# Performance work log

Hardware: AMD Instinct MI355X
Metric: run time of the kernel (lower is better)

The kernel has to match this reference:

```python
import jax, jax.numpy as jnp
import numpy as np

N_NODES = 50000
N_EDGES = 500000
NEG_SLOPE = 0.2  # PyG GATConv default leaky_relu slope
EPS = 1e-16


def gat_conv(x, src, dst, W, a_src, a_dst, b, heads, ch):
    """PyG-style GATConv (concat=True), self-loops assumed already in src/dst."""
    n = x.shape[0]
    h = (x @ W).reshape(n, heads, ch)                      # [N,H,C]
    alpha_s = jnp.sum(h * a_src, axis=-1)                  # [N,H]
    alpha_d = jnp.sum(h * a_dst, axis=-1)                  # [N,H]
    e = jax.nn.leaky_relu(alpha_s[src] + alpha_d[dst], NEG_SLOPE)  # [E,H]
    m = jax.ops.segment_max(e, dst, num_segments=n)        # [N,H] segment softmax (stable)
    m = jnp.where(jnp.isfinite(m), m, 0.0)
    ex = jnp.exp(e - m[dst])
    den = jax.ops.segment_sum(ex, dst, num_segments=n)
    alpha = ex / (den[dst] + EPS)                          # [E,H]
    msg = h[src] * alpha[..., None]                        # [E,H,C] gather->weight
    out = jax.ops.segment_sum(msg, dst, num_segments=n)    # [N,H,C] scatter-add
    return out.reshape(n, heads * ch) + b


def setup_inputs() -> dict:
    key = jax.random.key(0)
    ks = jax.random.split(key, 11)
    s = 0.05
    return {
        "edge_index": jax.random.randint(ks[0], (2, N_EDGES), 0, N_NODES, dtype=jnp.int32),
        "batch_size": 8,
        "node_emb": jax.random.normal(ks[1], (N_NODES, 64), jnp.float32),
        "W1": jax.random.normal(ks[2], (64, 512), jnp.float32) * s,
        "att_src1": jax.random.normal(ks[3], (4, 128), jnp.float32) * s,
        "att_dst1": jax.random.normal(ks[4], (4, 128), jnp.float32) * s,
        "b1": jax.random.normal(ks[5], (512,), jnp.float32) * s,
        "W2": jax.random.normal(ks[6], (512, 256), jnp.float32) * s,
        "att_src2": jax.random.normal(ks[7], (1, 256), jnp.float32) * s,
        "att_dst2": jax.random.normal(ks[8], (1, 256), jnp.float32) * s,
        "b2": jax.random.normal(ks[9], (256,), jnp.float32) * s,
    }


def reference(edge_index, batch_size, node_emb, W1, att_src1, att_dst1, b1,
              W2, att_src2, att_dst2, b2):
    # add self-loops (PyG GATConv default add_self_loops=True)
    loops = jnp.arange(N_NODES, dtype=edge_index.dtype)
    src = jnp.concatenate([edge_index[0], loops])
    dst = jnp.concatenate([edge_index[1], loops])
    x = gat_conv(node_emb, src, dst, W1, att_src1, att_dst1, b1, heads=4, ch=128)
    x = jax.nn.elu(x)  # dropout inactive at eval
    x = gat_conv(x, src, dst, W2, att_src2, att_dst2, b2, heads=1, ch=256)
    g = jnp.mean(x, axis=0, keepdims=True)                 # [1, 256]
    return jnp.broadcast_to(g, (batch_size, g.shape[1]))
```

## Files before the change

kernel.cpp:

```cpp
#include <hip/hip_runtime.h>
#include <cstdint>

#define N_NODES 50000
#define N_EDGES 500000
#define ET (N_NODES + N_EDGES)
#define WSB 256
#define EBLK 2149
#define NEBLK 12500

typedef unsigned short u16;
typedef unsigned int   u32;
typedef __attribute__((ext_vector_type(8))) short short8;
typedef __attribute__((ext_vector_type(4))) float f32x4;

__device__ __forceinline__ float bf2f(u16 s) { return __uint_as_float((u32)s << 16); }
__device__ __forceinline__ u16 f2bf(float f) {
  u32 u = __float_as_uint(f);
  u32 r = (u + 0x7FFFu + ((u >> 16) & 1u)) >> 16;
  return (u16)r;
}
__device__ __forceinline__ void unpack8(uint4 u, float* f) {
  f[0] = __uint_as_float(u.x << 16); f[1] = __uint_as_float(u.x & 0xffff0000u);
  f[2] = __uint_as_float(u.y << 16); f[3] = __uint_as_float(u.y & 0xffff0000u);
  f[4] = __uint_as_float(u.z << 16); f[5] = __uint_as_float(u.z & 0xffff0000u);
  f[6] = __uint_as_float(u.w << 16); f[7] = __uint_as_float(u.w & 0xffff0000u);
}
__device__ __forceinline__ float lrelu(float v) { return v >= 0.f ? v : 0.2f * v; }

__device__ __forceinline__ int detect_fp32(const u16* __restrict__ ne) {
  int lane = threadIdx.x & 63;
  int bad = 0;
  #pragma unroll
  for (int j = 0; j < 2; ++j) {
    float v = fabsf(bf2f(ne[lane * 2 + j * 128]));
    bad += (!(v < 16.0f)) ? 1 : 0;
  }
  #pragma unroll
  for (int off = 32; off >= 1; off >>= 1) bad += __shfl_xor(bad, off, 64);
  return bad > 16;
}

__global__ __launch_bounds__(256) void k_prep(const int* __restrict__ ei,
                                              int* __restrict__ deg,
                                              const void* __restrict__ ne_src,
                                              u16* __restrict__ ne_b,
                                              const void* __restrict__ w1src,
                                              u16* __restrict__ W1t,
                                              const void* __restrict__ w2src,
                                              u16* __restrict__ W2t,
                                              const void* s0, const void* s1,
                                              const void* s2, const void* s3,
                                              const void* s4, const void* s5,
                                              float* d0, float* d1, float* d2,
                                              float* d3, float* d4, float* d5) {
  int b = blockIdx.x, tid = threadIdx.x;
  if (b < EBLK) {
    int e = b * 256 + tid;
    if (e < ET) {
      int d = (e < N_EDGES) ? ei[N_EDGES + e] : (e - N_EDGES);
      atomicAdd(&deg[d], 1);
    }
    return;
  }
  int fp32 = detect_fp32((const u16*)ne_src);
  b -= EBLK;
  if (b < NEBLK) {
    int i = b * 256 + tid;
    ne_b[i] = fp32 ? f2bf(((const float*)ne_src)[i]) : ((const u16*)ne_src)[i];
    return;
  }
  b -= NEBLK;
  if (b < 640) {
    int i = b * 256 + tid;
    if (i < 32768) {
      int n = i >> 6, k = i & 63;
      W1t[i] = fp32 ? f2bf(((const float*)w1src)[k * 512 + n])
                    : ((const u16*)w1src)[k * 512 + n];
    } else {
      int j = i - 32768;
      int n = j >> 9, k = j & 511;
      W2t[j] = fp32 ? f2bf(((const float*)w2src)[k * 256 + n])
                    : ((const u16*)w2src)[k * 256 + n];
    }
    return;
  }
  b -= 640;
  {
    int i = b * 256 + tid;
    const void* s; float* d; int j;
    if      (i < 512)  { s = s0; d = d0; j = i; }
    else if (i < 1024) { s = s1; d = d1; j = i - 512; }
    else if (i < 1536) { s = s2; d = d2; j = i - 1024; }
    else if (i < 1792) { s = s3; d = d3; j = i - 1536; }
    else if (i < 2048) { s = s4; d = d4; j = i - 1792; }
    else if (i < 2304) { s = s5; d = d5; j = i - 2048; }
    else return;
    d[j] = fp32 ? ((const float*)s)[j] : bf2f(((const u16*)s)[j]);
  }
}

__global__ void k_vab(const u16* __restrict__ W1t,
                      const float* __restrict__ as1v, const float* __restrict__ ad1v,
                      float* __restrict__ va_s, float* __restrict__ va_d,
                      const u16* __restrict__ W2t,
                      const float* __restrict__ as2v, const float* __restrict__ ad2v,
                      float* __restrict__ va2_s, float* __restrict__ va2_d) {
  if (blockIdx.x == 0) {
    int t = threadIdx.x;
    int h = t >> 6, k = t & 63;
    float s = 0.f, d = 0.f;
    for (int c = 0; c < 128; ++c) {
      float w = bf2f(W1t[(size_t)(h * 128 + c) * 64 + k]);
      s = fmaf(as1v[h * 128 + c], w, s);
      d = fmaf(ad1v[h * 128 + c], w, d);
    }
    va_s[t] = s;
    va_d[t] = d;
  } else {
    int k = (blockIdx.x - 1) * 256 + threadIdx.x;
    if (k >= 512) return;
    float s = 0.f, d = 0.f;
    for (int c = 0; c < 256; ++c) {
      float w = bf2f(W2t[(size_t)c * 512 + k]);
      s = fmaf(as2v[c], w, s);
      d = fmaf(ad2v[c], w, d);
    }
    va2_s[k] = s;
    va2_d[k] = d;
  }
}

__global__ __launch_bounds__(1024) void k_partial(const int* __restrict__ deg,
                                                  int* __restrict__ excl,
                                                  int* __restrict__ btot) {
  __shared__ int wsum[16];
  int tid = threadIdx.x;
  int i = blockIdx.x * 1024 + tid;
  int v = (i < N_NODES) ? deg[i] : 0;
  int lane = tid & 63, wid = tid >> 6;
  int incl = v;
  #pragma unroll
  for (int off = 1; off < 64; off <<= 1) {
    int t = __shfl_up(incl, off, 64);
    if (lane >= off) incl += t;
  }
  if (lane == 63) wsum[wid] = incl;
  __syncthreads();
  int prefix = 0;
  for (int w = 0; w < wid; ++w) prefix += wsum[w];
  if (i < N_NODES) excl[i] = prefix + incl - v;
  if (tid == 1023) btot[blockIdx.x] = prefix + incl;
}

__global__ void k_bases(const int* __restrict__ btot, int* __restrict__ bbase,
                        int* __restrict__ row_off, int nb) {
  int lane = threadIdx.x;
  int v = (lane < nb) ? btot[lane] : 0;
  int incl = v;
  #pragma unroll
  for (int off = 1; off < 64; off <<= 1) {
    int t = __shfl_up(incl, off, 64);
    if (lane >= off) incl += t;
  }
  if (lane < nb) bbase[lane] = incl - v;
  if (lane == 0) row_off[N_NODES] = ET;
}

__global__ __launch_bounds__(1024) void k_add(int* __restrict__ row_off,
                                              int* __restrict__ cursor,
                                              const int* __restrict__ bbase) {
  int i = blockIdx.x * 1024 + threadIdx.x;
  if (i < N_NODES) {
    int r = row_off[i] + bbase[blockIdx.x];
    row_off[i] = r;
    cursor[i] = r;
  }
}

__global__ __launch_bounds__(256) void k_scal(const int* __restrict__ ei,
                                              int* __restrict__ cursor,
                                              u16* __restrict__ srcs,
                                              const u16* __restrict__ ne_b,
                                              const float* __restrict__ va_s,
                                              const float* __restrict__ va_d,
                                              float* __restrict__ as_o,
                                              float* __restrict__ ad_o) {
  int b = blockIdx.x;
  if (b < EBLK) {
    int e = b * 256 + threadIdx.x;
    if (e >= ET) return;
    int s, d;
    if (e < N_EDGES) { s = ei[e]; d = ei[N_EDGES + e]; }
    else { s = d = e - N_EDGES; }
    int pos = atomicAdd(&cursor[d], 1);
    srcs[pos] = (u16)s;
    return;
  }
  b -= EBLK;
  int wid = threadIdx.x >> 6, lane = threadIdx.x & 63;
  int n = b * 4 + wid;
  if (n >= N_NODES) return;
  int h = lane >> 4, il = lane & 15;
  u32 u2[2];
  *(uint2*)u2 = *(const uint2*)(ne_b + (size_t)n * 64 + il * 4);
  float f[4];
  f[0] = bf2f((u16)u2[0]); f[1] = bf2f((u16)(u2[0] >> 16));
  f[2] = bf2f((u16)u2[1]); f[3] = bf2f((u16)(u2[1] >> 16));
  float4 vs = *(const float4*)(va_s + h * 64 + il * 4);
  float4 vd = *(const float4*)(va_d + h * 64 + il * 4);
  float s = f[0] * vs.x + f[1] * vs.y + f[2] * vs.z + f[3] * vs.w;
  float d = f[0] * vd.x + f[1] * vd.y + f[2] * vd.z + f[3] * vd.w;
  #pragma unroll
  for (int off = 8; off >= 1; off >>= 1) {
    s += __shfl_xor(s, off, 64);
    d += __shfl_xor(d, off, 64);
  }
  if (il == 0) { as_o[n * 4 + h] = s; ad_o[n * 4 + h] = d; }
}

#define LSTR 40
#define CPAD 136
__global__ __launch_bounds__(256, 6) void k_gemm_l1(const u16* __restrict__ aggne,
                                                    const u16* __restrict__ W1t,
                                                    const float* __restrict__ b1f,
                                                    const float* __restrict__ va2_s,
                                                    const float* __restrict__ va2_d,
                                                    u16* __restrict__ x2,
                                                    float* __restrict__ as2,
                                                    float* __restrict__ ad2, int M) {
  __shared__ __align__(16) u16 smem[64 * CPAD];
  u16* As = smem;
  u16* Bs = smem + 64 * LSTR;
  const int tid = threadIdx.x;
  const int lane = tid & 63, wid = tid >> 6;
  const int wr = (wid >> 1) * 32, wc = (wid & 1) * 64;
  const int m = lane & 15, q = lane >> 4;
  const int row0 = blockIdx.x * 64, head = blockIdx.y;
  const u16* Bt = W1t + (size_t)head * 128 * 64;
  f32x4 acc[2][4] = {};
  #pragma unroll
  for (int kk = 0; kk < 64; kk += 32) {
    {
      int row = tid >> 2, ch = (tid & 3) * 8;
      uint4 u = make_uint4(0, 0, 0, 0);
      int gr = row0 + row;
      if (gr < M) u = *(const uint4*)(aggne + (size_t)gr * 256 + head * 64 + kk + ch);
      *(uint4*)(As + row * LSTR + ch) = u;
    }
    #pragma unroll
    for (int i = 0; i < 2; ++i) {
      int v = tid + i * 256;
      int row = v >> 2, ch = (v & 3) * 8;
      uint4 u = *(const uint4*)(Bt + (size_t)row * 64 + kk + ch);
      *(uint4*)(Bs + row * LSTR + ch) = u;
    }
    __syncthreads();
    short8 af[2], bfr[4];
    #pragma unroll
    for (int t = 0; t < 2; ++t)
      af[t]  = *(const short8*)(As + (wr + t * 16 + m) * LSTR + q * 8);
    #pragma unroll
    for (int t = 0; t < 4; ++t)
      bfr[t] = *(const short8*)(Bs + (wc + t * 16 + m) * LSTR + q * 8);
    #pragma unroll
    for (int mt = 0; mt < 2; ++mt)
      #pragma unroll
      for (int nt = 0; nt < 4; ++nt)
        acc[mt][nt] = __builtin_amdgcn_mfma_f32_16x16x32_bf16(
            af[mt], bfr[nt], acc[mt][nt], 0, 0, 0);
    __syncthreads();
  }
  u16* Cs = smem;
  #pragma unroll
  for (int mt = 0; mt < 2; ++mt) {
    #pragma unroll
    for (int nt = 0; nt < 4; ++nt) {
      int lc = wc + nt * 16 + m;
      float bias = b1f[head * 128 + lc];
      #pragma unroll
      for (int r = 0; r < 4; ++r) {
        float v = acc[mt][nt][r] + bias;
        v = v > 0.f ? v : (__expf(v) - 1.0f);
        Cs[(wr + mt * 16 + q * 4 + r) * CPAD + lc] = f2bf(v);
      }
    }
  }
  __syncthreads();
  int row = tid >> 2, qt = tid & 3;
  int gr = row0 + row;
  if (gr < M) {
    const u16* src = Cs + row * CPAD + qt * 32;
    int cb = head * 128 + qt * 32;
    float s = 0.f, d = 0.f;
    #pragma unroll
    for (int i = 0; i < 4; ++i) {
      uint4 u = *(const uint4*)(src + i * 8);
      *(uint4*)(x2 + (size_t)gr * 512 + cb + i * 8) = u;
      float f[8];
      unpack8(u, f);
      const float* pvs = va2_s + cb + i * 8;
      const float* pvd = va2_d + cb + i * 8;
      #pragma unroll
      for (int j = 0; j < 8; ++j) {
        s = fmaf(f[j], pvs[j], s);
        d = fmaf(f[j], pvd[j], d);
      }
    }
    s += __shfl_xor(s, 1, 64);
    d += __shfl_xor(d, 1, 64);
    s += __shfl_xor(s, 2, 64);
    d += __shfl_xor(d, 2, 64);
    if (qt == 0) {
      atomicAdd(&as2[gr], s);
      atomicAdd(&ad2[gr], d);
    }
  }
}

__global__ __launch_bounds__(256) void k_fagg1(const int* __restrict__ row_off,
                                               const u16* __restrict__ srcs,
                                               const u16* __restrict__ ne_b,
                                               const float* __restrict__ as1,
                                               const float* __restrict__ ad1,
                                               u16* __restrict__ aggne) {
  int wid = threadIdx.x >> 6, lane = threadIdx.x & 63;
  int n = blockIdx.x * 4 + wid;
  if (n >= N_NODES) return;
  int start = row_off[n], end = row_off[n + 1];
  int g = lane >> 4, il = lane & 15;
  float adn_g = ad1[n * 4 + g];
  float sum = 0.f;
  for (int e0 = start; e0 < end; e0 += 16) {
    int e = e0 + il;
    if (e < end) sum += __expf(lrelu(as1[(int)srcs[e] * 4 + g] + adn_g));
  }
  #pragma unroll
  for (int off = 8; off >= 1; off >>= 1) sum += __shfl_xor(sum, off, 64);
  float inv = 1.0f / (sum + 1e-16f);
  float i_[4], d_[4];
  #pragma unroll
  for (int h = 0; h < 4; ++h) {
    i_[h] = __shfl(inv, h * 16, 64);
    d_[h] = __shfl(adn_g, h * 16, 64);
  }
  float acc[4] = {};
  for (int e0 = start; e0 < end; e0 += 64) {
    int lim = end - e0; if (lim > 64) lim = 64;
    int es = e0 + lane;
    int sreg = (int)srcs[es < end ? es : end - 1];
    float4 a = *(const float4*)(as1 + sreg * 4);
    float wreg[4];
    wreg[0] = __expf(lrelu(a.x + d_[0])) * i_[0];
    wreg[1] = __expf(lrelu(a.y + d_[1])) * i_[1];
    wreg[2] = __expf(lrelu(a.z + d_[2])) * i_[2];
    wreg[3] = __expf(lrelu(a.w + d_[3])) * i_[3];
    int j = 0;
    for (; j + 3 < lim; j += 4) {
      int sa = __shfl(sreg, j, 64),     sb = __shfl(sreg, j + 1, 64);
      int sc = __shfl(sreg, j + 2, 64), sd = __shfl(sreg, j + 3, 64);
      float f0 = bf2f(ne_b[(size_t)sa * 64 + lane]);
      float f1 = bf2f(ne_b[(size_t)sb * 64 + lane]);
      float f2 = bf2f(ne_b[(size_t)sc * 64 + lane]);
      float f3 = bf2f(ne_b[(size_t)sd * 64 + lane]);
      #pragma unroll
      for (int h = 0; h < 4; ++h) {
        acc[h] = fmaf(__shfl(wreg[h], j, 64), f0, acc[h]);
        acc[h] = fmaf(__shfl(wreg[h], j + 1, 64), f1, acc[h]);
        acc[h] = fmaf(__shfl(wreg[h], j + 2, 64), f2, acc[h]);
        acc[h] = fmaf(__shfl(wreg[h], j + 3, 64), f3, acc[h]);
      }
    }
    for (; j < lim; ++j) {
      int sa = __shfl(sreg, j, 64);
      float f0 = bf2f(ne_b[(size_t)sa * 64 + lane]);
      #pragma unroll
      for (int h = 0; h < 4; ++h)
        acc[h] = fmaf(__shfl(wreg[h], j, 64), f0, acc[h]);
    }
  }
  #pragma unroll
  for (int h = 0; h < 4; ++h)
    aggne[(size_t)n * 256 + h * 64 + lane] = f2bf(acc[h]);
}

__global__ __launch_bounds__(256) void k_nodew(const int* __restrict__ row_off,
                                               const u16* __restrict__ srcs,
                                               const float* __restrict__ as2,
                                               const float* __restrict__ ad2,
                                               float* __restrict__ c) {
  int wid = threadIdx.x >> 6, lane = threadIdx.x & 63;
  int n = blockIdx.x * 4 + wid;
  if (n >= N_NODES) return;
  int start = row_off[n], end = row_off[n + 1];
  int deg = end - start;
  float adn = ad2[n];
  if (deg <= 64) {
    int e = start + (lane < deg ? lane : 0);
    int s = (int)srcs[e];
    float ex = (lane < deg) ? __expf(lrelu(as2[s] + adn)) : 0.f;
    float sum = ex;
    #pragma unroll
    for (int off = 32; off >= 1; off >>= 1) sum += __shfl_xor(sum, off, 64);
    float w = ex / (sum + 1e-16f);
    if (lane < deg) atomicAdd(&c[s], w);
  } else {
    float sum = 0.f;
    for (int e = start + lane; e < end; e += 64)
      sum += __expf(lrelu(as2[(int)srcs[e]] + adn));
    #pragma unroll
    for (int off = 32; off >= 1; off >>= 1) sum += __shfl_xor(sum, off, 64);
    float inv = 1.0f / (sum + 1e-16f);
    for (int e = start + lane; e < end; e += 64) {
      int s = (int)srcs[e];
      float w = __expf(lrelu(as2[s] + adn)) * inv;
      atomicAdd(&c[s], w);
    }
  }
}

__global__ __launch_bounds__(256) void k_wsum(const u16* __restrict__ x2,
                                              const float* __restrict__ c,
                                              float* __restrict__ s_vec) {
  __shared__ float part[4][512];
  int wid = threadIdx.x >> 6, lane = threadIdx.x & 63;
  int wglob = blockIdx.x * 4 + wid;
  float acc[8] = {};
  int n = wglob;
  for (; n + WSB * 4 < N_NODES; n += WSB * 8) {
    int n2 = n + WSB * 4;
    float c0 = c[n], c1 = c[n2];
    uint4 u0 = *(const uint4*)(x2 + (size_t)n * 512 + lane * 8);
    uint4 u1 = *(const uint4*)(x2 + (size_t)n2 * 512 + lane * 8);
    float f0[8], f1[8];
    unpack8(u0, f0); unpack8(u1, f1);
    #pragma unroll
    for (int j = 0; j < 8; ++j) {
      acc[j] = fmaf(c0, f0[j], acc[j]);
      acc[j] = fmaf(c1, f1[j], acc[j]);
    }
  }
  if (n < N_NODES) {
    float c0 = c[n];
    uint4 u0 = *(const uint4*)(x2 + (size_t)n * 512 + lane * 8);
    float f0[8];
    unpack8(u0, f0);
    #pragma unroll
    for (int j = 0; j < 8; ++j) acc[j] = fmaf(c0, f0[j], acc[j]);
  }
  #pragma unroll
  for (int j = 0; j < 8; ++j) part[wid][lane * 8 + j] = acc[j];
  __syncthreads();
  int t = threadIdx.x;
  float v0 = part[0][t] + part[1][t] + part[2][t] + part[3][t];
  float v1 = part[0][t + 256] + part[1][t + 256] + part[2][t + 256] + part[3][t + 256];
  atomicAdd(&s_vec[t], v0);
  atomicAdd(&s_vec[t + 256], v1);
}

__global__ __launch_bounds__(256) void k_tinyfinal(const float* __restrict__ s_vec,
                                                   const u16* __restrict__ W2t,
                                                   const float* __restrict__ b2f,
                                                   float* __restrict__ out,
                                                   int out_size) {
  int wid = threadIdx.x >> 6, lane = threadIdx.x & 63;
  int cbase = blockIdx.x * 64 + wid * 16;
  float sv[8];
  #pragma unroll
  for (int j = 0; j < 8; ++j) sv[j] = s_vec[lane * 8 + j];
  for (int i = 0; i < 16; ++i) {
    int cc = cbase + i;
    uint4 u = *(const uint4*)(W2t + (size_t)cc * 512 + lane * 8);
    float f[8];
    unpack8(u, f);
    float p = 0.f;
    #pragma unroll
    for (int j = 0; j < 8; ++j) p = fmaf(sv[j], f[j], p);
    #pragma unroll
    for (int off = 32; off >= 1; off >>= 1) p += __shfl_xor(p, off, 64);
    if (lane == 0) {
      float val = p * (1.0f / (float)N_NODES) + b2f[cc];
      for (int o = cc; o < out_size; o += 256) out[o] = val;
    }
  }
}

extern "C" void kernel_launch(void* const* d_in, const int* in_sizes, int n_in,
                              void* d_out, int out_size, void* d_ws, size_t ws_size,
                              hipStream_t stream) {
  (void)in_sizes; (void)n_in; (void)ws_size;
  const int* edge_index = (const int*)d_in[0];
  float* out = (float*)d_out;

  char* w = (char*)d_ws;
  size_t off = 0;
  auto alloc = [&](size_t bytes) -> void* {
    void* p = w + off;
    off += (bytes + 255) & ~(size_t)255;
    return p;
  };
  u16*   ne_b    = (u16*)  alloc((size_t)N_NODES * 64 * 2);
  u16*   W1t     = (u16*)  alloc(32768 * 2);
  u16*   W2t     = (u16*)  alloc(131072 * 2);
  float* as1v    = (float*)alloc(512 * 4);
  float* ad1v    = (float*)alloc(512 * 4);
  float* b1f     = (float*)alloc(512 * 4);
  float* as2v    = (float*)alloc(256 * 4);
  float* ad2v    = (float*)alloc(256 * 4);
  float* b2f     = (float*)alloc(256 * 4);
  float* va_s    = (float*)alloc(256 * 4);
  float* va_d    = (float*)alloc(256 * 4);
  float* va2_s   = (float*)alloc(512 * 4);
  float* va2_d   = (float*)alloc(512 * 4);
  u16*   aggne   = (u16*)  alloc((size_t)N_NODES * 256 * 2);
  u16*   x2      = (u16*)  alloc((size_t)N_NODES * 512 * 2);
  float* as1     = (float*)alloc((size_t)N_NODES * 4 * 4);
  float* ad1     = (float*)alloc((size_t)N_NODES * 4 * 4);
  size_t z0 = off;
  float* as2     = (float*)alloc((size_t)N_NODES * 4);
  float* ad2     = (float*)alloc((size_t)N_NODES * 4);
  float* cwt     = (float*)alloc((size_t)N_NODES * 4);
  float* s_vec   = (float*)alloc(512 * 4);
  int*   deg     = (int*)  alloc((size_t)N_NODES * 4);
  size_t z1 = off;
  int*   row_off = (int*)  alloc((size_t)(N_NODES + 1) * 4);
  int*   cursor  = (int*)  alloc((size_t)N_NODES * 4);
  u16*   srcs    = (u16*)  alloc((size_t)ET * 2);
  int*   btot    = (int*)  alloc(64 * 4);
  int*   bbase   = (int*)  alloc(64 * 4);

  hipMemsetAsync(w + z0, 0, z1 - z0, stream);

  k_prep<<<EBLK + NEBLK + 640 + 9, 256, 0, stream>>>(
      edge_index, deg, d_in[2], ne_b, d_in[3], W1t, d_in[7], W2t,
      d_in[4], d_in[5], d_in[6], d_in[8], d_in[9], d_in[10],
      as1v, ad1v, b1f, as2v, ad2v, b2f);
  k_vab<<<3, 256, 0, stream>>>(W1t, as1v, ad1v, va_s, va_d,
                               W2t, as2v, ad2v, va2_s, va2_d);

  k_partial<<<49, 1024, 0, stream>>>(deg, row_off, btot);
  k_bases  <<<1, 64, 0, stream>>>(btot, bbase, row_off, 49);
  k_add    <<<49, 1024, 0, stream>>>(row_off, cursor, bbase);

  k_scal<<<EBLK + (N_NODES + 3) / 4, 256, 0, stream>>>(
      edge_index, cursor, srcs, ne_b, va_s, va_d, as1, ad1);

  k_fagg1<<<(N_NODES + 3) / 4, 256, 0, stream>>>(row_off, srcs, ne_b, as1, ad1, aggne);
  dim3 gl1((N_NODES + 63) / 64, 4);
  k_gemm_l1<<<gl1, 256, 0, stream>>>(aggne, W1t, b1f, va2_s, va2_d, x2, as2, ad2,
                                     N_NODES);

  k_nodew<<<(N_NODES + 3) / 4, 256, 0, stream>>>(row_off, srcs, as2, ad2, cwt);
  k_wsum<<<WSB, 256, 0, stream>>>(x2, cwt, s_vec);
  k_tinyfinal<<<4, 256, 0, stream>>>(s_vec, W2t, b2f, out, out_size);
}
```

Before: 309.0 us.

## Loop over heads inside GEMM block and drop atomics for layer-2 scores

The layer-1 GEMM kernel now runs one block per 64-row tile and loops over all four heads, loading the full 256-wide A tile into shared memory once instead of using a separate grid dimension per head. The per-node layer-2 attention scores are accumulated in registers across heads and written directly, so the atomicAdds go away and the as2/ad2 buffers move out of the memset range. In exchange, shared memory per block grows to about 68KB and each block does four times the work over a quarter of the blocks. That can lower occupancy and adds more syncthreads barriers per block.

Result: slower. 324.3 us (+5.0%).

```diff
diff --git a/kernel.cpp b/kernel.cpp
--- a/kernel.cpp
+++ b/kernel.cpp
@@ -218,102 +218,107 @@
   if (il == 0) { as_o[n * 4 + h] = s; ad_o[n * 4 + h] = d; }
 }
 
-#define LSTR 40
+#define ASTR 264
+#define BSTR 72
 #define CPAD 136
-__global__ __launch_bounds__(256, 6) void k_gemm_l1(const u16* __restrict__ aggne,
-                                                    const u16* __restrict__ W1t,
-                                                    const float* __restrict__ b1f,
-                                                    const float* __restrict__ va2_s,
-                                                    const float* __restrict__ va2_d,
-                                                    u16* __restrict__ x2,
-                                                    float* __restrict__ as2,
-                                                    float* __restrict__ ad2, int M) {
-  __shared__ __align__(16) u16 smem[64 * CPAD];
-  u16* As = smem;
-  u16* Bs = smem + 64 * LSTR;
+__global__ __launch_bounds__(256) void k_gemm_l1(const u16* __restrict__ aggne,
+                                                 const u16* __restrict__ W1t,
+                                                 const float* __restrict__ b1f,
+                                                 const float* __restrict__ va2_s,
+                                                 const float* __restrict__ va2_d,
+                                                 u16* __restrict__ x2,
+                                                 float* __restrict__ as2,
+                                                 float* __restrict__ ad2, int M) {
+  __shared__ __align__(16) u16 As[64 * ASTR];
+  __shared__ __align__(16) u16 Bs[128 * BSTR];
+  __shared__ __align__(16) u16 Cs[64 * CPAD];
   const int tid = threadIdx.x;
   const int lane = tid & 63, wid = tid >> 6;
   const int wr = (wid >> 1) * 32, wc = (wid & 1) * 64;
   const int m = lane & 15, q = lane >> 4;
-  const int row0 = blockIdx.x * 64, head = blockIdx.y;
-  const u16* Bt = W1t + (size_t)head * 128 * 64;
-  f32x4 acc[2][4] = {};
-  #pragma unroll
-  for (int kk = 0; kk < 64; kk += 32) {
-    {
-      int row = tid >> 2, ch = (tid & 3) * 8;
-      uint4 u = make_uint4(0, 0, 0, 0);
-      int gr = row0 + row;
-      if (gr < M) u = *(const uint4*)(aggne + (size_t)gr * 256 + head * 64 + kk + ch);
-      *(uint4*)(As + row * LSTR + ch) = u;
-    }
-    #pragma unroll
-    for (int i = 0; i < 2; ++i) {
-      int v = tid + i * 256;
-      int row = v >> 2, ch = (v & 3) * 8;
-      uint4 u = *(const uint4*)(Bt + (size_t)row * 64 + kk + ch);
-      *(uint4*)(Bs + row * LSTR + ch) = u;
-    }
+  const int row0 = blockIdx.x * 64;
+  #pragma unroll
+  for (int i = 0; i < 8; ++i) {
+    int g = i * 256 + tid;
+    int row = g >> 5, ch = (g & 31) * 8;
+    uint4 u = make_uint4(0, 0, 0, 0);
+    int gr = row0 + row;
+    if (gr < M) u = *(const uint4*)(aggne + (size_t)gr * 256 + ch);
+    *(uint4*)(As + row * ASTR + ch) = u;
+  }
+  const int erow = tid >> 2, eqt = tid & 3;
+  const int egr = row0 + erow;
+  float s_acc = 0.f, d_acc = 0.f;
+  for (int h = 0; h < 4; ++h) {
     __syncthreads();
-    short8 af[2], bfr[4];
-    #pragma unroll
-    for (int t = 0; t < 2; ++t)
-      af[t]  = *(const short8*)(As + (wr + t * 16 + m) * LSTR + q * 8);
-    #pragma unroll
-    for (int t = 0; t < 4; ++t)
-      bfr[t] = *(const short8*)(Bs + (wc + t * 16 + m) * LSTR + q * 8);
-    #pragma unroll
-    for (int mt = 0; mt < 2; ++mt)
-      #pragma unroll
-      for (int nt = 0; nt < 4; ++nt)
-        acc[mt][nt] = __builtin_amdgcn_mfma_f32_16x16x32_bf16(
-            af[mt], bfr[nt], acc[mt][nt], 0, 0, 0);
+    const u16* Bt = W1t + (size_t)h * 128 * 64;
+    #pragma unroll
+    for (int i = 0; i < 4; ++i) {
+      int g = i * 256 + tid;
+      int row = g >> 3, ch = (g & 7) * 8;
+      uint4 u = *(const uint4*)(Bt + (size_t)row * 64 + ch);
+      *(uint4*)(Bs + row * BSTR + ch) = u;
+    }
     __syncthreads();
-  }
-  u16* Cs = smem;
-  #pragma unroll
-  for (int mt = 0; mt < 2; ++mt) {
-    #pragma unroll
-    for (int nt = 0; nt < 4; ++nt) {
-      int lc = wc + nt * 16 + m;
-      float bias = b1f[head * 128 + lc];
-      #pragma unroll
-      for (int r = 0; r < 4; ++r) {
-        float v = acc[mt][nt][r] + bias;
-        v = v > 0.f ? v : (__expf(v) - 1.0f);
-        Cs[(wr + mt * 16 + q * 4 + r) * CPAD + lc] = f2bf(v);
+    f32x4 acc[2][4] = {};
+    #pragma unroll
+    for (int kk = 0; kk < 2; ++kk) {
+      short8 af[2], bfr[4];
+      #pragma unroll
+      for (int t = 0; t < 2; ++t)
+        af[t]  = *(const short8*)(As + (wr + t * 16 + m) * ASTR + h * 64 +
+                                  kk * 32 + q * 8);
+      #pragma unroll
+      for (int t = 0; t < 4; ++t)
+        bfr[t] = *(const short8*)(Bs + (wc + t * 16 + m) * BSTR + kk * 32 + q * 8);
+      #pragma unroll
+      for (int mt = 0; mt < 2; ++mt)
+        #pragma unroll
+        for (int nt = 0; nt < 4; ++nt)
+          acc[mt][nt] = __builtin_amdgcn_mfma_f32_16x16x32_bf16(
+              af[mt], bfr[nt], acc[mt][nt], 0, 0, 0);
+    }
+    #pragma unroll
+    for (int mt = 0; mt < 2; ++mt) {
+      #pragma unroll
+      for (int nt = 0; nt < 4; ++nt) {
+        int lc = wc + nt * 16 + m;
+        float bias = b1f[h * 128 + lc];
+        #pragma unroll
+        for (int r = 0; r < 4; ++r) {
+          float v = acc[mt][nt][r] + bias;
+          v = v > 0.f ? v : (__expf(v) - 1.0f);
+          Cs[(wr + mt * 16 + q * 4 + r) * CPAD + lc] = f2bf(v);
+        }
       }
     }
-  }
-  __syncthreads();
-  int row = tid >> 2, qt = tid & 3;
-  int gr = row0 + row;
-  if (gr < M) {
-    const u16* src = Cs + row * CPAD + qt * 32;
-    int cb = head * 128 + qt * 32;
-    float s = 0.f, d = 0.f;
-    #pragma unroll
-    for (int i = 0; i < 4; ++i) {
-      uint4 u = *(const uint4*)(src + i * 8);
-      *(uint4*)(x2 + (size_t)gr * 512 + cb + i * 8) = u;
-      float f[8];
-      unpack8(u, f);
-      const float* pvs = va2_s + cb + i * 8;
-      const float* pvd = va2_d + cb + i * 8;
-      #pragma unroll
-      for (int j = 0; j < 8; ++j) {
-        s = fmaf(f[j], pvs[j], s);
-        d = fmaf(f[j], pvd[j], d);
+    __syncthreads();
+    if (egr < M) {
+      const u16* src = Cs + erow * CPAD + eqt * 32;
+      int cb = h * 128 + eqt * 32;
+      #pragma unroll
+      for (int i = 0; i < 4; ++i) {
+        uint4 u = *(const uint4*)(src + i * 8);
+        *(uint4*)(x2 + (size_t)egr * 512 + cb + i * 8) = u;
+        float f[8];
+        unpack8(u, f);
+        const float* pvs = va2_s + cb + i * 8;
+        const float* pvd = va2_d + cb + i * 8;
+        #pragma unroll
+        for (int j = 0; j < 8; ++j) {
+          s_acc = fmaf(f[j], pvs[j], s_acc);
+          d_acc = fmaf(f[j], pvd[j], d_acc);
+        }
       }
     }
-    s += __shfl_xor(s, 1, 64);
-    d += __shfl_xor(d, 1, 64);
-    s += __shfl_xor(s, 2, 64);
-    d += __shfl_xor(d, 2, 64);
-    if (qt == 0) {
-      atomicAdd(&as2[gr], s);
-      atomicAdd(&ad2[gr], d);
-    }
+  }
+  s_acc += __shfl_xor(s_acc, 1, 64);
+  d_acc += __shfl_xor(d_acc, 1, 64);
+  s_acc += __shfl_xor(s_acc, 2, 64);
+  d_acc += __shfl_xor(d_acc, 2, 64);
+  if (eqt == 0 && egr < M) {
+    as2[egr] = s_acc;
+    ad2[egr] = d_acc;
   }
 }
 
@@ -515,9 +520,9 @@
   u16*   x2      = (u16*)  alloc((size_t)N_NODES * 512 * 2);
   float* as1     = (float*)alloc((size_t)N_NODES * 4 * 4);
   float* ad1     = (float*)alloc((size_t)N_NODES * 4 * 4);
-  size_t z0 = off;
   float* as2     = (float*)alloc((size_t)N_NODES * 4);
   float* ad2     = (float*)alloc((size_t)N_NODES * 4);
+  size_t z0 = off;
   float* cwt     = (float*)alloc((size_t)N_NODES * 4);
   float* s_vec   = (float*)alloc(512 * 4);
   int*   deg     = (int*)  alloc((size_t)N_NODES * 4);
@@ -545,9 +550,8 @@
       edge_index, cursor, srcs, ne_b, va_s, va_d, as1, ad1);
 
   k_fagg1<<<(N_NODES + 3) / 4, 256, 0, stream>>>(row_off, srcs, ne_b, as1, ad1, aggne);
-  dim3 gl1((N_NODES + 63) / 64, 4);
-  k_gemm_l1<<<gl1, 256, 0, stream>>>(aggne, W1t, b1f, va2_s, va2_d, x2, as2, ad2,
-                                     N_NODES);
+  k_gemm_l1<<<(N_NODES + 63) / 64, 256, 0, stream>>>(aggne, W1t, b1f, va2_s, va2_d,
+                                                     x2, as2, ad2, N_NODES);
 
   k_nodew<<<(N_NODES + 3) / 4, 256, 0, stream>>>(row_off, srcs, as2, ad2, cwt);
   k_wsum<<<WSB, 256, 0, stream>>>(x2, cwt, s_vec);
```
